# Kernel tuning notes

Measured on AMD Instinct MI355X. Metric: run time of the kernel, lower is better.

The kernel has to match this reference:

```python
import jax, jax.numpy as jnp
import numpy as np
from jax import lax

HIDDEN = 1024
SEQ_NUM = 2048
SEQ_LEN = 10  # hard-coded by input_seq.view(-1, 1, 10) in the torch module


def setup_inputs() -> dict:
    key = jax.random.key(0)
    ks = jax.random.split(key, 7)
    s = 1.0 / np.sqrt(HIDDEN)  # torch RNN/Linear default init scale
    return {
        "input_seq": jax.random.normal(ks[0], (SEQ_NUM, SEQ_LEN), dtype=jnp.float32),
        "W_ih": jax.random.uniform(ks[1], (HIDDEN, 1), jnp.float32, -s, s),
        "b_ih": jax.random.uniform(ks[2], (HIDDEN,), jnp.float32, -s, s),
        "W_hh": jax.random.uniform(ks[3], (HIDDEN, HIDDEN), jnp.float32, -s, s),
        "b_hh": jax.random.uniform(ks[4], (HIDDEN,), jnp.float32, -s, s),
        "W_out": jax.random.uniform(ks[5], (1, HIDDEN), jnp.float32, -s, s),
        "b_out": jax.random.uniform(ks[6], (1,), jnp.float32, -s, s),
    }


def reference(input_seq, W_ih, b_ih, W_hh, b_hh, W_out, b_out):
    # Torch module feeds each scalar of input_seq (viewed as [seqNum,1,10])
    # through nn.RNN one step at a time, carrying hidden_cell across ALL
    # scalars, and applies Linear to the hidden state at every step.
    # h' = tanh(x * w_ih + b_ih + W_hh @ h + b_hh); y = W_out @ h' + b_out
    w_ih = W_ih[:, 0]  # input_size == 1
    xs = input_seq.reshape(-1)  # [T] scalar timesteps, T = seqNum*10

    def step(h, x):
        h_new = jnp.tanh(x * w_ih + b_ih + W_hh @ h + b_hh)
        y = W_out @ h_new + b_out  # [1]
        return h_new, y[0]

    h0 = jnp.zeros((HIDDEN,), dtype=input_seq.dtype)
    _, ys = lax.scan(step, h0, xs)
    return ys.reshape(SEQ_NUM, 1, SEQ_LEN)
```

## Files before the change

kernel.cpp:

```cpp
#include <hip/hip_runtime.h>
#include <math.h>


#define H      1024
#define TSTEPS 20480
#define BLOCK  256
#define WARM   64
#define WGSPC  16

typedef unsigned int uint;
typedef float f32x4 __attribute__((ext_vector_type(4)));

#define HDATA_BYTES ((size_t)64 * 2 * H * sizeof(float))

__device__ __forceinline__ uint f2bf(float f) {
    uint u = __float_as_uint(f);
    return (u + 0x7fffu + ((u >> 16) & 1u)) >> 16;
}

__global__ __launch_bounds__(BLOCK, 1)
void rnn_r22(const float* __restrict__ xs, const float* __restrict__ W_ih,
             const float* __restrict__ b_ih, const float* __restrict__ W_hh,
             const float* __restrict__ b_hh, const float* __restrict__ W_out,
             const float* __restrict__ b_out, float* __restrict__ y,
             float* __restrict__ hdata, uint* __restrict__ ctrl,
             int coop, int ilv, int chunk)
{
    const int tid  = threadIdx.x;
    const int bid  = blockIdx.x;
    const int wave = tid >> 6;
    const int lane = tid & 63;

    __shared__ uint  sW[64][512];
    __shared__ uint  sR[256];
    __shared__ int   sA[3];
    __shared__ float sY[4][4][8];

    uint* rcount = ctrl;
    uint* abortf = ctrl + 16;
    uint* roster = ctrl + 64;
    uint* flbase = ctrl + 1024;

    int group, slot; bool fastm;
    if (coop) {
        uint xcc = __builtin_amdgcn_s_getreg(20 | (31 << 11)) & 7u;
        if (tid == 0) {
            __hip_atomic_store(&roster[bid], xcc, __ATOMIC_RELAXED, __HIP_MEMORY_SCOPE_AGENT);
            asm volatile("s_waitcnt vmcnt(0)" ::: "memory");
            atomicAdd(rcount, 1u);
            while (__hip_atomic_load(rcount, __ATOMIC_RELAXED, __HIP_MEMORY_SCOPE_AGENT) < 256u)
                __builtin_amdgcn_s_sleep(2);
        }
        __syncthreads();
        sR[tid] = __hip_atomic_load(&roster[tid], __ATOMIC_RELAXED, __HIP_MEMORY_SCOPE_AGENT);
        __syncthreads();
        if (tid == 0) {
            int cnt[8] = {0,0,0,0,0,0,0,0};
            int myrank = 0, myx = 0;
            for (int b = 0; b < 256; ++b) {
                int x = (int)(sR[b] & 7u);
                int r = cnt[x]++;
                if (b == bid) { myrank = r; myx = x; }
            }
            int pre[9]; pre[0] = 0;
            for (int x = 0; x < 8; ++x) pre[x + 1] = pre[x] + cnt[x];
            int gidx = pre[myx] + myrank;
            int gr = gidx >> 4, sl = gidx & 15;
            int lo = gr << 4, hi = lo + 16, fok = 0;
            for (int x = 0; x < 8; ++x)
                if (pre[x] <= lo && hi <= pre[x + 1]) fok = 1;
            sA[0] = gr; sA[1] = sl; sA[2] = fok;
        }
        __syncthreads();
        group = sA[0]; slot = sA[1]; fastm = (sA[2] != 0);
    } else {
        group = bid / WGSPC; slot = bid % WGSPC; fastm = false;
    }

    uint* abortp = abortf + group;
    const int wic     = slot * 4 + wave;
    const int rowbase = slot * 64 + wave * 16;
    const int rowwg   = slot * 64;
    const int ck0     = group * ilv;

    for (int idx = tid; idx < 64 * 512; idx += BLOCK) {
        const int r = idx >> 9, p = idx & 511;
        const float2 w = *(const float2*)&W_hh[(size_t)(rowwg + r) * H + 2 * p];
        sW[r][p] = f2bf(w.x) | (f2bf(w.y) << 16);
    }
    __syncthreads();

    const int myrow = rowbase + (lane & 15);
    const float wih_s = W_ih[myrow];
    const float cb_s  = b_ih[myrow] + b_hh[myrow];

    f32x4 wo4[4];
    #pragma unroll
    for (int q = 0; q < 4; ++q)
        wo4[q] = *(const f32x4*)&W_out[256 * q + 4 * lane];
    const float bo = b_out[0];

    int ns[4], t0c[4];
    #pragma unroll
    for (int k = 0; k < 4; ++k) {
        const int ck = ck0 + k;
        const int w_ = (k < ilv && ck) ? WARM : 0;
        ns[k]  = (k < ilv) ? chunk + w_ : 0;
        t0c[k] = ck * chunk - w_;
    }

    f32x4 hrv[4][4] = {};
    float lv0[4] = {0,0,0,0}, lv1[4] = {0,0,0,0};
    uint  lastflag[4] = {0,0,0,0};
    float xcur[4] = {0,0,0,0};
    #pragma unroll
    for (int k = 0; k < 4; ++k)
        if (k < ilv) xcur[k] = xs[t0c[k]];

    auto demote = [&]() {
        #pragma unroll
        for (int k = 0; k < 4; ++k) {
            if (k >= ilv) continue;
            float* hbk = hdata + (size_t)(ck0 + k) * 2 * H;
            float* q0 = hbk + rowbase + (lane & 15);
            float* q1 = q0 + H;
            if (lane < 16) {
                asm volatile("global_store_dword %0, %1, off sc0 sc1"
                             :: "v"(q0), "v"(lv0[k]) : "memory");
                asm volatile("global_store_dword %0, %1, off sc0 sc1"
                             :: "v"(q1), "v"(lv1[k]) : "memory");
            }
            asm volatile("s_waitcnt vmcnt(0)" ::: "memory");
            if (lane == 0)
                asm volatile("global_store_dword %0, %1, off sc0 sc1"
                             :: "v"(flbase + (ck0 + k) * 64 + wic), "v"(lastflag[k]) : "memory");
        }
        asm volatile("s_waitcnt vmcnt(0)" ::: "memory");
        if (lane == 0)
            asm volatile("global_store_dword %0, %1, off sc0 sc1"
                         :: "v"(abortp), "v"(1u) : "memory");
        asm volatile("s_waitcnt vmcnt(0)" ::: "memory");
        fastm = false;
    };

    auto abort_set = [&]() -> bool {
        uint ab;
        asm volatile("global_load_dword %0, %1, off sc0 sc1\n\ts_waitcnt vmcnt(0)"
                     : "=v"(ab) : "v"(abortp) : "memory");
        return __any(ab != 0u);
    };

    auto poll_load_t = [&](int ck, int lt, float* out) {
        const uint* fa = flbase + ck * 64 + lane;
        const uint tt = (uint)lt;
        uint fails = 0;
        for (;;) {
            uint f;
            if (fastm)
                asm volatile("global_load_dword %0, %1, off sc0\n\ts_waitcnt vmcnt(0)"
                             : "=v"(f) : "v"(fa) : "memory");
            else
                asm volatile("global_load_dword %0, %1, off sc0 sc1\n\ts_waitcnt vmcnt(0)"
                             : "=v"(f) : "v"(fa) : "memory");
            if (__all(f >= tt)) break;
            ++fails;
            if (fastm) {
                if ((fails & 63u) == 0u) {
                    if (abort_set() || fails > 8192u) demote();
                }
                __builtin_amdgcn_s_sleep(1);
            } else {
                __builtin_amdgcn_s_sleep(8);
            }
        }
        const float* a = hdata + (size_t)ck * 2 * H + (size_t)(lt & 1) * H + 4 * lane;
        f32x4 A, B, C, D;
        if (fastm)
            asm volatile(
                "global_load_dwordx4 %0, %4, off sc0\n\t"
                "global_load_dwordx4 %1, %4, off offset:1024 sc0\n\t"
                "global_load_dwordx4 %2, %4, off offset:2048 sc0\n\t"
                "global_load_dwordx4 %3, %4, off offset:3072 sc0\n\t"
                "s_waitcnt vmcnt(0)"
                : "=&v"(A), "=&v"(B), "=&v"(C), "=&v"(D) : "v"(a) : "memory");
        else
            asm volatile(
                "global_load_dwordx4 %0, %4, off sc0 sc1\n\t"
                "global_load_dwordx4 %1, %4, off offset:1024 sc0 sc1\n\t"
                "global_load_dwordx4 %2, %4, off offset:2048 sc0 sc1\n\t"
                "global_load_dwordx4 %3, %4, off offset:3072 sc0 sc1\n\t"
                "s_waitcnt vmcnt(0)"
                : "=&v"(A), "=&v"(B), "=&v"(C), "=&v"(D) : "v"(a) : "memory");
        #pragma unroll
        for (int e = 0; e < 4; ++e) {
            out[e] = A[e]; out[4 + e] = B[e]; out[8 + e] = C[e]; out[12 + e] = D[e];
        }
    };

    auto reduce16 = [&](const float* z) -> float {
        float s0,s1,s2,s3,s4,s5,s6,s7;
        {
            const bool b = (lane & 1) != 0;
            s0 = (b ? z[ 1] : z[ 0]) + __shfl_xor(b ? z[ 0] : z[ 1], 1);
            s1 = (b ? z[ 3] : z[ 2]) + __shfl_xor(b ? z[ 2] : z[ 3], 1);
            s2 = (b ? z[ 5] : z[ 4]) + __shfl_xor(b ? z[ 4] : z[ 5], 1);
            s3 = (b ? z[ 7] : z[ 6]) + __shfl_xor(b ? z[ 6] : z[ 7], 1);
            s4 = (b ? z[ 9] : z[ 8]) + __shfl_xor(b ? z[ 8] : z[ 9], 1);
            s5 = (b ? z[11] : z[10]) + __shfl_xor(b ? z[10] : z[11], 1);
            s6 = (b ? z[13] : z[12]) + __shfl_xor(b ? z[12] : z[13], 1);
            s7 = (b ? z[15] : z[14]) + __shfl_xor(b ? z[14] : z[15], 1);
        }
        float t0_,t1_,t2_,t3_;
        {
            const bool b = (lane & 2) != 0;
            t0_ = (b ? s1 : s0) + __shfl_xor(b ? s0 : s1, 2);
            t1_ = (b ? s3 : s2) + __shfl_xor(b ? s2 : s3, 2);
            t2_ = (b ? s5 : s4) + __shfl_xor(b ? s4 : s5, 2);
            t3_ = (b ? s7 : s6) + __shfl_xor(b ? s6 : s7, 2);
        }
        float u0_,u1_;
        {
            const bool b = (lane & 4) != 0;
            u0_ = (b ? t1_ : t0_) + __shfl_xor(b ? t0_ : t1_, 4);
            u1_ = (b ? t3_ : t2_) + __shfl_xor(b ? t2_ : t3_, 4);
        }
        float zr;
        {
            const bool b = (lane & 8) != 0;
            zr = (b ? u1_ : u0_) + __shfl_xor(b ? u0_ : u1_, 8);
        }
        zr += __shfl_xor(zr, 16);
        zr += __shfl_xor(zr, 32);
        return zr;
    };

    auto reduce16x2 = [&](const float* za, const float* zb, float& ra, float& rb) {
        const bool b1 = (lane & 1) != 0;
        float sa0 = (b1 ? za[ 1] : za[ 0]) + __shfl_xor(b1 ? za[ 0] : za[ 1], 1);
        float sb0 = (b1 ? zb[ 1] : zb[ 0]) + __shfl_xor(b1 ? zb[ 0] : zb[ 1], 1);
        float sa1 = (b1 ? za[ 3] : za[ 2]) + __shfl_xor(b1 ? za[ 2] : za[ 3], 1);
        float sb1 = (b1 ? zb[ 3] : zb[ 2]) + __shfl_xor(b1 ? zb[ 2] : zb[ 3], 1);
        float sa2 = (b1 ? za[ 5] : za[ 4]) + __shfl_xor(b1 ? za[ 4] : za[ 5], 1);
        float sb2 = (b1 ? zb[ 5] : zb[ 4]) + __shfl_xor(b1 ? zb[ 4] : zb[ 5], 1);
        float sa3 = (b1 ? za[ 7] : za[ 6]) + __shfl_xor(b1 ? za[ 6] : za[ 7], 1);
        float sb3 = (b1 ? zb[ 7] : zb[ 6]) + __shfl_xor(b1 ? zb[ 6] : zb[ 7], 1);
        float sa4 = (b1 ? za[ 9] : za[ 8]) + __shfl_xor(b1 ? za[ 8] : za[ 9], 1);
        float sb4 = (b1 ? zb[ 9] : zb[ 8]) + __shfl_xor(b1 ? zb[ 8] : zb[ 9], 1);
        float sa5 = (b1 ? za[11] : za[10]) + __shfl_xor(b1 ? za[10] : za[11], 1);
        float sb5 = (b1 ? zb[11] : zb[10]) + __shfl_xor(b1 ? zb[10] : zb[11], 1);
        float sa6 = (b1 ? za[13] : za[12]) + __shfl_xor(b1 ? za[12] : za[13], 1);
        float sb6 = (b1 ? zb[13] : zb[12]) + __shfl_xor(b1 ? zb[12] : zb[13], 1);
        float sa7 = (b1 ? za[15] : za[14]) + __shfl_xor(b1 ? za[14] : za[15], 1);
        float sb7 = (b1 ? zb[15] : zb[14]) + __shfl_xor(b1 ? zb[14] : zb[15], 1);
        const bool b2 = (lane & 2) != 0;
        float ta0 = (b2 ? sa1 : sa0) + __shfl_xor(b2 ? sa0 : sa1, 2);
        float tb0 = (b2 ? sb1 : sb0) + __shfl_xor(b2 ? sb0 : sb1, 2);
        float ta1 = (b2 ? sa3 : sa2) + __shfl_xor(b2 ? sa2 : sa3, 2);
        float tb1 = (b2 ? sb3 : sb2) + __shfl_xor(b2 ? sb2 : sb3, 2);
        float ta2 = (b2 ? sa5 : sa4) + __shfl_xor(b2 ? sa4 : sa5, 2);
        float tb2 = (b2 ? sb5 : sb4) + __shfl_xor(b2 ? sb4 : sb5, 2);
        float ta3 = (b2 ? sa7 : sa6) + __shfl_xor(b2 ? sa6 : sa7, 2);
        float tb3 = (b2 ? sb7 : sb6) + __shfl_xor(b2 ? sb6 : sb7, 2);
        const bool b4 = (lane & 4) != 0;
        float ua0 = (b4 ? ta1 : ta0) + __shfl_xor(b4 ? ta0 : ta1, 4);
        float ub0 = (b4 ? tb1 : tb0) + __shfl_xor(b4 ? tb0 : tb1, 4);
        float ua1 = (b4 ? ta3 : ta2) + __shfl_xor(b4 ? ta2 : ta3, 4);
        float ub1 = (b4 ? tb3 : tb2) + __shfl_xor(b4 ? tb2 : tb3, 4);
        const bool b8 = (lane & 8) != 0;
        float va = (b8 ? ua1 : ua0) + __shfl_xor(b8 ? ua0 : ua1, 8);
        float vb = (b8 ? ub1 : ub0) + __shfl_xor(b8 ? ub0 : ub1, 8);
        va += __shfl_xor(va, 16);
        vb += __shfl_xor(vb, 16);
        va += __shfl_xor(va, 32);
        vb += __shfl_xor(vb, 32);
        ra = va; rb = vb;
    };

    const int nstep_max = chunk + ((ilv > 1 || group) ? WARM : 0);

    #pragma unroll 1
    for (int it = 0; it < nstep_max; ++it) {
        if (fastm && (it & 31) == 1) {
            if (abort_set()) demote();
        }

        float hv[4] = {0, 0, 0, 0};
        #pragma unroll
        for (int kp = 0; kp < 2; ++kp) {
            const int ka = 2 * kp, kb = 2 * kp + 1;
            const bool doa = (ka < ilv) && (it < ns[ka]);
            const bool dob = (kb < ilv) && (it < ns[kb]);
            if (!doa && !dob) continue;
            float za[16], zb[16];
            #pragma unroll
            for (int r = 0; r < 16; ++r) {
                const uint2* wrow = (const uint2*)&sW[wave * 16 + r][2 * lane];
                float a = 0.0f, b = 0.0f;
                #pragma unroll
                for (int q = 0; q < 4; ++q) {
                    const uint2 u = wrow[q * 64];
                    const float w0 = __uint_as_float(u.x << 16);
                    const float w1 = __uint_as_float(u.x & 0xffff0000u);
                    const float w2 = __uint_as_float(u.y << 16);
                    const float w3 = __uint_as_float(u.y & 0xffff0000u);
                    a = fmaf(w0, hrv[ka][q][0], a);
                    b = fmaf(w0, hrv[kb][q][0], b);
                    a = fmaf(w1, hrv[ka][q][1], a);
                    b = fmaf(w1, hrv[kb][q][1], b);
                    a = fmaf(w2, hrv[ka][q][2], a);
                    b = fmaf(w2, hrv[kb][q][2], b);
                    a = fmaf(w3, hrv[ka][q][3], a);
                    b = fmaf(w3, hrv[kb][q][3], b);
                }
                za[r] = a; zb[r] = b;
            }
            float zra, zrb;
            reduce16x2(za, zb, zra, zrb);
            const float va = fmaf(xcur[ka], wih_s, cb_s + zra);
            const float vb = fmaf(xcur[kb], wih_s, cb_s + zrb);
            const float ha = tanhf(va);
            const float hb = tanhf(vb);
            if (doa) hv[ka] = ha;
            if (dob) hv[kb] = hb;
        }

        const int par = (it + 1) & 1;
        #pragma unroll
        for (int k = 0; k < 4; ++k) {
            if (k >= ilv || it >= ns[k]) continue;
            float* dst = hdata + (size_t)((ck0 + k) * 2 + par) * H + rowbase + (lane & 15);
            if (lane < 16) {
                if (fastm)
                    asm volatile("global_store_dword %0, %1, off"
                                 :: "v"(dst), "v"(hv[k]) : "memory");
                else
                    asm volatile("global_store_dword %0, %1, off sc0 sc1"
                                 :: "v"(dst), "v"(hv[k]) : "memory");
            }
        }
        asm volatile("s_waitcnt vmcnt(0)" ::: "memory");
        #pragma unroll
        for (int k = 0; k < 4; ++k) {
            if (k >= ilv || it >= ns[k]) continue;
            const uint nf = (uint)(it + 1);
            if (lane == 0) {
                if (fastm)
                    asm volatile("global_store_dword %0, %1, off"
                                 :: "v"(flbase + (ck0 + k) * 64 + wic), "v"(nf) : "memory");
                else
                    asm volatile("global_store_dword %0, %1, off sc0 sc1"
                                 :: "v"(flbase + (ck0 + k) * 64 + wic), "v"(nf) : "memory");
            }
            if (par == 0) lv0[k] = hv[k]; else lv1[k] = hv[k];
            lastflag[k] = nf;
        }

        #pragma unroll
        for (int k = 0; k < 4; ++k) {
            if (k >= ilv || it >= ns[k]) continue;
            const int warm_k = (ck0 + k) ? WARM : 0;
            if (wic == (it & 63) && it >= warm_k + 1) {
                float acc = 0.0f;
                #pragma unroll
                for (int q = 0; q < 4; ++q) {
                    acc = fmaf(wo4[q][0], hrv[k][q][0], acc);
                    acc = fmaf(wo4[q][1], hrv[k][q][1], acc);
                    acc = fmaf(wo4[q][2], hrv[k][q][2], acc);
                    acc = fmaf(wo4[q][3], hrv[k][q][3], acc);
                }
                #pragma unroll
                for (int off = 32; off > 0; off >>= 1)
                    acc += __shfl_xor(acc, off);
                if (lane == 0) {
                    if (coop) sY[wave][k][it >> 6] = acc + bo;
                    else      y[t0c[k] + it - 1] = acc + bo;
                }
            }
            if (it + 1 < ns[k]) xcur[k] = xs[t0c[k] + it + 1];
        }

        if (ilv == 4) {
            uint tg0 = (it + 1 < ns[0]) ? (uint)(it + 1) : 0u;
            uint tg1 = (it + 1 < ns[1]) ? (uint)(it + 1) : 0u;
            uint tg2 = (it + 1 < ns[2]) ? (uint)(it + 1) : 0u;
            uint tg3 = (it + 1 < ns[3]) ? (uint)(it + 1) : 0u;
            if (tg0 | tg1 | tg2 | tg3) {
                const uint* fa = flbase + ck0 * 64 + lane;
                uint fails = 0;
                for (;;) {
                    uint f0, f1, f2, f3;
                    if (fastm)
                        asm volatile(
                            "global_load_dword %0, %4, off sc0\n\t"
                            "global_load_dword %1, %4, off offset:256 sc0\n\t"
                            "global_load_dword %2, %4, off offset:512 sc0\n\t"
                            "global_load_dword %3, %4, off offset:768 sc0\n\t"
                            "s_waitcnt vmcnt(0)"
                            : "=&v"(f0), "=&v"(f1), "=&v"(f2), "=&v"(f3)
                            : "v"(fa) : "memory");
                    else
                        asm volatile(
                            "global_load_dword %0, %4, off sc0 sc1\n\t"
                            "global_load_dword %1, %4, off offset:256 sc0 sc1\n\t"
                            "global_load_dword %2, %4, off offset:512 sc0 sc1\n\t"
                            "global_load_dword %3, %4, off offset:768 sc0 sc1\n\t"
                            "s_waitcnt vmcnt(0)"
                            : "=&v"(f0), "=&v"(f1), "=&v"(f2), "=&v"(f3)
                            : "v"(fa) : "memory");
                    bool ok = (f0 >= tg0) & (f1 >= tg1) & (f2 >= tg2) & (f3 >= tg3);
                    if (__all(ok)) break;
                    ++fails;
                    if (fastm) {
                        if ((fails & 63u) == 0u) {
                            if (abort_set() || fails > 8192u) demote();
                        }
                        __builtin_amdgcn_s_sleep(1);
                    } else {
                        __builtin_amdgcn_s_sleep(8);
                    }
                }
                const float* a0p = hdata + (size_t)(ck0 * 2 + par) * H + 4 * lane;
                const float* a1p = a0p + 2 * H;
                const float* a2p = a0p + 4 * H;
                const float* a3p = a0p + 6 * H;
                if (fastm)
                    asm volatile(
                        "global_load_dwordx4 %0, %16, off sc0\n\t"
                        "global_load_dwordx4 %1, %16, off offset:1024 sc0\n\t"
                        "global_load_dwordx4 %2, %16, off offset:2048 sc0\n\t"
                        "global_load_dwordx4 %3, %16, off offset:3072 sc0\n\t"
                        "global_load_dwordx4 %4, %17, off sc0\n\t"
                        "global_load_dwordx4 %5, %17, off offset:1024 sc0\n\t"
                        "global_load_dwordx4 %6, %17, off offset:2048 sc0\n\t"
                        "global_load_dwordx4 %7, %17, off offset:3072 sc0\n\t"
                        "global_load_dwordx4 %8, %18, off sc0\n\t"
                        "global_load_dwordx4 %9, %18, off offset:1024 sc0\n\t"
                        "global_load_dwordx4 %10, %18, off offset:2048 sc0\n\t"
                        "global_load_dwordx4 %11, %18, off offset:3072 sc0\n\t"
                        "global_load_dwordx4 %12, %19, off sc0\n\t"
                        "global_load_dwordx4 %13, %19, off offset:1024 sc0\n\t"
                        "global_load_dwordx4 %14, %19, off offset:2048 sc0\n\t"
                        "global_load_dwordx4 %15, %19, off offset:3072 sc0\n\t"
                        "s_waitcnt vmcnt(0)"
                        : "=&v"(hrv[0][0]), "=&v"(hrv[0][1]), "=&v"(hrv[0][2]), "=&v"(hrv[0][3]),
                          "=&v"(hrv[1][0]), "=&v"(hrv[1][1]), "=&v"(hrv[1][2]), "=&v"(hrv[1][3]),
                          "=&v"(hrv[2][0]), "=&v"(hrv[2][1]), "=&v"(hrv[2][2]), "=&v"(hrv[2][3]),
                          "=&v"(hrv[3][0]), "=&v"(hrv[3][1]), "=&v"(hrv[3][2]), "=&v"(hrv[3][3])
                        : "v"(a0p), "v"(a1p), "v"(a2p), "v"(a3p) : "memory");
                else
                    asm volatile(
                        "global_load_dwordx4 %0, %16, off sc0 sc1\n\t"
                        "global_load_dwordx4 %1, %16, off offset:1024 sc0 sc1\n\t"
                        "global_load_dwordx4 %2, %16, off offset:2048 sc0 sc1\n\t"
                        "global_load_dwordx4 %3, %16, off offset:3072 sc0 sc1\n\t"
                        "global_load_dwordx4 %4, %17, off sc0 sc1\n\t"
                        "global_load_dwordx4 %5, %17, off offset:1024 sc0 sc1\n\t"
                        "global_load_dwordx4 %6, %17, off offset:2048 sc0 sc1\n\t"
                        "global_load_dwordx4 %7, %17, off offset:3072 sc0 sc1\n\t"
                        "global_load_dwordx4 %8, %18, off sc0 sc1\n\t"
                        "global_load_dwordx4 %9, %18, off offset:1024 sc0 sc1\n\t"
                        "global_load_dwordx4 %10, %18, off offset:2048 sc0 sc1\n\t"
                        "global_load_dwordx4 %11, %18, off offset:3072 sc0 sc1\n\t"
                        "global_load_dwordx4 %12, %19, off sc0 sc1\n\t"
                        "global_load_dwordx4 %13, %19, off offset:1024 sc0 sc1\n\t"
                        "global_load_dwordx4 %14, %19, off offset:2048 sc0 sc1\n\t"
                        "global_load_dwordx4 %15, %19, off offset:3072 sc0 sc1\n\t"
                        "s_waitcnt vmcnt(0)"
                        : "=&v"(hrv[0][0]), "=&v"(hrv[0][1]), "=&v"(hrv[0][2]), "=&v"(hrv[0][3]),
                          "=&v"(hrv[1][0]), "=&v"(hrv[1][1]), "=&v"(hrv[1][2]), "=&v"(hrv[1][3]),
                          "=&v"(hrv[2][0]), "=&v"(hrv[2][1]), "=&v"(hrv[2][2]), "=&v"(hrv[2][3]),
                          "=&v"(hrv[3][0]), "=&v"(hrv[3][1]), "=&v"(hrv[3][2]), "=&v"(hrv[3][3])
                        : "v"(a0p), "v"(a1p), "v"(a2p), "v"(a3p) : "memory");
            }
        } else {
            if (it + 1 < ns[0]) {
                float out[16];
                poll_load_t(ck0, it + 1, out);
                #pragma unroll
                for (int q = 0; q < 4; ++q)
                    #pragma unroll
                    for (int e = 0; e < 4; ++e)
                        hrv[0][q][e] = out[4 * q + e];
            }
        }
    }

    if (coop) {
        #pragma unroll
        for (int k = 0; k < 4; ++k) {
            if (k >= ilv) continue;
            const int warm_k = (ck0 + k) ? WARM : 0;
            #pragma unroll 1
            for (int kk = 0; kk < 8; ++kk) {
                const int it = (kk << 6) + wic;
                if (it >= warm_k + 1 && it < ns[k] && lane == 0)
                    y[t0c[k] + it - 1] = sY[wave][k][kk];
            }
        }
    }

    if (slot == 0 && wave == 0) {
        #pragma unroll
        for (int k = 0; k < 4; ++k) {
            if (k >= ilv) continue;
            float out[16];
            poll_load_t(ck0 + k, ns[k], out);
            float acc = 0.0f;
            #pragma unroll
            for (int q = 0; q < 4; ++q) {
                acc = fmaf(wo4[q][0], out[4 * q + 0], acc);
                acc = fmaf(wo4[q][1], out[4 * q + 1], acc);
                acc = fmaf(wo4[q][2], out[4 * q + 2], acc);
                acc = fmaf(wo4[q][3], out[4 * q + 3], acc);
            }
            #pragma unroll
            for (int off = 32; off > 0; off >>= 1)
                acc += __shfl_xor(acc, off);
            if (lane == 0) y[t0c[k] + ns[k] - 1] = acc + bo;
        }
    }
}

extern "C" void kernel_launch(void* const* d_in, const int* in_sizes, int n_in,
                              void* d_out, int out_size, void* d_ws, size_t ws_size,
                              hipStream_t stream) {
    const float* xs    = (const float*)d_in[0];
    const float* W_ih  = (const float*)d_in[1];
    const float* b_ih  = (const float*)d_in[2];
    const float* W_hh  = (const float*)d_in[3];
    const float* b_hh  = (const float*)d_in[4];
    const float* W_out = (const float*)d_in[5];
    const float* b_out = (const float*)d_in[6];
    float* y = (float*)d_out;

    const size_t ctrl_bytes = 24576;
    const size_t need = HDATA_BYTES + ctrl_bytes;
    int use_coop = (ws_size >= need) ? 1 : 0;

    float* hdata = (float*)d_ws;
    uint*  ctrl  = (uint*)((char*)d_ws +
                           (use_coop ? HDATA_BYTES
                                     : (size_t)4 * 2 * H * sizeof(float)));

    (void)hipMemsetAsync(d_ws, 0,
                         use_coop ? need
                                  : (size_t)4 * 2 * H * sizeof(float) + ctrl_bytes,
                         stream);

    if (use_coop) {
        int coop = 1, ilv = 4, chunk = TSTEPS / 64;
        void* args[] = { (void*)&xs, (void*)&W_ih, (void*)&b_ih, (void*)&W_hh,
                         (void*)&b_hh, (void*)&W_out, (void*)&b_out, (void*)&y,
                         (void*)&hdata, (void*)&ctrl,
                         (void*)&coop, (void*)&ilv, (void*)&chunk };
        hipError_t e = hipLaunchCooperativeKernel((const void*)rnn_r22,
                                                  dim3(256), dim3(BLOCK),
                                                  args, 0, stream);
        if (e != hipSuccess) use_coop = 0;
    }
    if (!use_coop) {
        rnn_r22<<<4 * WGSPC, BLOCK, 0, stream>>>(
            xs, W_ih, b_ih, W_hh, b_hh, W_out, b_out, y,
            hdata, ctrl, 0, 1, TSTEPS / 4);
    }
}
```

Before: 4.996 ms.

## Double waves per workgroup so each wave owns eight hidden rows

Raises the block size from 256 to 512 threads, giving 8 waves per workgroup, each computing 8 hidden rows instead of 16. The per-wave matvec and shuffle reduction shrink accordingly, shortening the serial critical path of each recurrent step. In exchange there are twice as many per-wave ready flags, so every poll reads two flag words per lane per chunk, and the flag and control region is enlarged to hold them.

```diff
diff --git a/kernel.cpp b/kernel.cpp
--- a/kernel.cpp
+++ b/kernel.cpp
@@ -4,7 +4,7 @@
 
 #define H      1024
 #define TSTEPS 20480
-#define BLOCK  256
+#define BLOCK  512
 #define WARM   64
 #define WGSPC  16
 
@@ -12,6 +12,7 @@
 typedef float f32x4 __attribute__((ext_vector_type(4)));
 
 #define HDATA_BYTES ((size_t)64 * 2 * H * sizeof(float))
+#define CTRL_BYTES  ((size_t)40960)
 
 __device__ __forceinline__ uint f2bf(float f) {
     uint u = __float_as_uint(f);
@@ -19,7 +20,7 @@
 }
 
 __global__ __launch_bounds__(BLOCK, 1)
-void rnn_r22(const float* __restrict__ xs, const float* __restrict__ W_ih,
+void rnn_r23(const float* __restrict__ xs, const float* __restrict__ W_ih,
              const float* __restrict__ b_ih, const float* __restrict__ W_hh,
              const float* __restrict__ b_hh, const float* __restrict__ W_out,
              const float* __restrict__ b_out, float* __restrict__ y,
@@ -34,7 +35,7 @@
     __shared__ uint  sW[64][512];
     __shared__ uint  sR[256];
     __shared__ int   sA[3];
-    __shared__ float sY[4][4][8];
+    __shared__ float sY[8][4][4];
 
     uint* rcount = ctrl;
     uint* abortf = ctrl + 16;
@@ -52,7 +53,8 @@
                 __builtin_amdgcn_s_sleep(2);
         }
         __syncthreads();
-        sR[tid] = __hip_atomic_load(&roster[tid], __ATOMIC_RELAXED, __HIP_MEMORY_SCOPE_AGENT);
+        if (tid < 256)
+            sR[tid] = __hip_atomic_load(&roster[tid], __ATOMIC_RELAXED, __HIP_MEMORY_SCOPE_AGENT);
         __syncthreads();
         if (tid == 0) {
             int cnt[8] = {0,0,0,0,0,0,0,0};
@@ -78,8 +80,8 @@
     }
 
     uint* abortp = abortf + group;
-    const int wic     = slot * 4 + wave;
-    const int rowbase = slot * 64 + wave * 16;
+    const int wic     = slot * 8 + wave;
+    const int rowbase = slot * 64 + wave * 8;
     const int rowwg   = slot * 64;
     const int ck0     = group * ilv;
 
@@ -90,7 +92,7 @@
     }
     __syncthreads();
 
-    const int myrow = rowbase + (lane & 15);
+    const int myrow = rowbase + (lane & 7);
     const float wih_s = W_ih[myrow];
     const float cb_s  = b_ih[myrow] + b_hh[myrow];
 
@@ -122,9 +124,9 @@
         for (int k = 0; k < 4; ++k) {
             if (k >= ilv) continue;
             float* hbk = hdata + (size_t)(ck0 + k) * 2 * H;
-            float* q0 = hbk + rowbase + (lane & 15);
+            float* q0 = hbk + rowbase + (lane & 7);
             float* q1 = q0 + H;
-            if (lane < 16) {
+            if (lane < 8) {
                 asm volatile("global_store_dword %0, %1, off sc0 sc1"
                              :: "v"(q0), "v"(lv0[k]) : "memory");
                 asm volatile("global_store_dword %0, %1, off sc0 sc1"
@@ -133,7 +135,7 @@
             asm volatile("s_waitcnt vmcnt(0)" ::: "memory");
             if (lane == 0)
                 asm volatile("global_store_dword %0, %1, off sc0 sc1"
-                             :: "v"(flbase + (ck0 + k) * 64 + wic), "v"(lastflag[k]) : "memory");
+                             :: "v"(flbase + (ck0 + k) * 128 + wic), "v"(lastflag[k]) : "memory");
         }
         asm volatile("s_waitcnt vmcnt(0)" ::: "memory");
         if (lane == 0)
@@ -151,18 +153,22 @@
     };
 
     auto poll_load_t = [&](int ck, int lt, float* out) {
-        const uint* fa = flbase + ck * 64 + lane;
+        const uint* fa = flbase + ck * 128 + lane;
         const uint tt = (uint)lt;
         uint fails = 0;
         for (;;) {
-            uint f;
+            uint f0, f1;
             if (fastm)
-                asm volatile("global_load_dword %0, %1, off sc0\n\ts_waitcnt vmcnt(0)"
-                             : "=v"(f) : "v"(fa) : "memory");
+                asm volatile("global_load_dword %0, %2, off sc0\n\t"
+                             "global_load_dword %1, %2, off offset:256 sc0\n\t"
+                             "s_waitcnt vmcnt(0)"
+                             : "=&v"(f0), "=&v"(f1) : "v"(fa) : "memory");
             else
-                asm volatile("global_load_dword %0, %1, off sc0 sc1\n\ts_waitcnt vmcnt(0)"
-                             : "=v"(f) : "v"(fa) : "memory");
-            if (__all(f >= tt)) break;
+                asm volatile("global_load_dword %0, %2, off sc0 sc1\n\t"
+                             "global_load_dword %1, %2, off offset:256 sc0 sc1\n\t"
+                             "s_waitcnt vmcnt(0)"
+                             : "=&v"(f0), "=&v"(f1) : "v"(fa) : "memory");
+            if (__all((f0 >= tt) & (f1 >= tt))) break;
             ++fails;
             if (fastm) {
                 if ((fails & 63u) == 0u) {
@@ -197,78 +203,26 @@
         }
     };
 
-    auto reduce16 = [&](const float* z) -> float {
-        float s0,s1,s2,s3,s4,s5,s6,s7;
-        {
-            const bool b = (lane & 1) != 0;
-            s0 = (b ? z[ 1] : z[ 0]) + __shfl_xor(b ? z[ 0] : z[ 1], 1);
-            s1 = (b ? z[ 3] : z[ 2]) + __shfl_xor(b ? z[ 2] : z[ 3], 1);
-            s2 = (b ? z[ 5] : z[ 4]) + __shfl_xor(b ? z[ 4] : z[ 5], 1);
-            s3 = (b ? z[ 7] : z[ 6]) + __shfl_xor(b ? z[ 6] : z[ 7], 1);
-            s4 = (b ? z[ 9] : z[ 8]) + __shfl_xor(b ? z[ 8] : z[ 9], 1);
-            s5 = (b ? z[11] : z[10]) + __shfl_xor(b ? z[10] : z[11], 1);
-            s6 = (b ? z[13] : z[12]) + __shfl_xor(b ? z[12] : z[13], 1);
-            s7 = (b ? z[15] : z[14]) + __shfl_xor(b ? z[14] : z[15], 1);
-        }
-        float t0_,t1_,t2_,t3_;
-        {
-            const bool b = (lane & 2) != 0;
-            t0_ = (b ? s1 : s0) + __shfl_xor(b ? s0 : s1, 2);
-            t1_ = (b ? s3 : s2) + __shfl_xor(b ? s2 : s3, 2);
-            t2_ = (b ? s5 : s4) + __shfl_xor(b ? s4 : s5, 2);
-            t3_ = (b ? s7 : s6) + __shfl_xor(b ? s6 : s7, 2);
-        }
-        float u0_,u1_;
-        {
-            const bool b = (lane & 4) != 0;
-            u0_ = (b ? t1_ : t0_) + __shfl_xor(b ? t0_ : t1_, 4);
-            u1_ = (b ? t3_ : t2_) + __shfl_xor(b ? t2_ : t3_, 4);
-        }
-        float zr;
-        {
-            const bool b = (lane & 8) != 0;
-            zr = (b ? u1_ : u0_) + __shfl_xor(b ? u0_ : u1_, 8);
-        }
-        zr += __shfl_xor(zr, 16);
-        zr += __shfl_xor(zr, 32);
-        return zr;
-    };
-
-    auto reduce16x2 = [&](const float* za, const float* zb, float& ra, float& rb) {
+    auto reduce8x2 = [&](const float* za, const float* zb, float& ra, float& rb) {
         const bool b1 = (lane & 1) != 0;
-        float sa0 = (b1 ? za[ 1] : za[ 0]) + __shfl_xor(b1 ? za[ 0] : za[ 1], 1);
-        float sb0 = (b1 ? zb[ 1] : zb[ 0]) + __shfl_xor(b1 ? zb[ 0] : zb[ 1], 1);
-        float sa1 = (b1 ? za[ 3] : za[ 2]) + __shfl_xor(b1 ? za[ 2] : za[ 3], 1);
-        float sb1 = (b1 ? zb[ 3] : zb[ 2]) + __shfl_xor(b1 ? zb[ 2] : zb[ 3], 1);
-        float sa2 = (b1 ? za[ 5] : za[ 4]) + __shfl_xor(b1 ? za[ 4] : za[ 5], 1);
-        float sb2 = (b1 ? zb[ 5] : zb[ 4]) + __shfl_xor(b1 ? zb[ 4] : zb[ 5], 1);
-        float sa3 = (b1 ? za[ 7] : za[ 6]) + __shfl_xor(b1 ? za[ 6] : za[ 7], 1);
-        float sb3 = (b1 ? zb[ 7] : zb[ 6]) + __shfl_xor(b1 ? zb[ 6] : zb[ 7], 1);
-        float sa4 = (b1 ? za[ 9] : za[ 8]) + __shfl_xor(b1 ? za[ 8] : za[ 9], 1);
-        float sb4 = (b1 ? zb[ 9] : zb[ 8]) + __shfl_xor(b1 ? zb[ 8] : zb[ 9], 1);
-        float sa5 = (b1 ? za[11] : za[10]) + __shfl_xor(b1 ? za[10] : za[11], 1);
-        float sb5 = (b1 ? zb[11] : zb[10]) + __shfl_xor(b1 ? zb[10] : zb[11], 1);
-        float sa6 = (b1 ? za[13] : za[12]) + __shfl_xor(b1 ? za[12] : za[13], 1);
-        float sb6 = (b1 ? zb[13] : zb[12]) + __shfl_xor(b1 ? zb[12] : zb[13], 1);
-        float sa7 = (b1 ? za[15] : za[14]) + __shfl_xor(b1 ? za[14] : za[15], 1);
-        float sb7 = (b1 ? zb[15] : zb[14]) + __shfl_xor(b1 ? zb[14] : zb[15], 1);
+        float sa0 = (b1 ? za[1] : za[0]) + __shfl_xor(b1 ? za[0] : za[1], 1);
+        float sb0 = (b1 ? zb[1] : zb[0]) + __shfl_xor(b1 ? zb[0] : zb[1], 1);
+        float sa1 = (b1 ? za[3] : za[2]) + __shfl_xor(b1 ? za[2] : za[3], 1);
+        float sb1 = (b1 ? zb[3] : zb[2]) + __shfl_xor(b1 ? zb[2] : zb[3], 1);
+        float sa2 = (b1 ? za[5] : za[4]) + __shfl_xor(b1 ? za[4] : za[5], 1);
+        float sb2 = (b1 ? zb[5] : zb[4]) + __shfl_xor(b1 ? zb[4] : zb[5], 1);
+        float sa3 = (b1 ? za[7] : za[6]) + __shfl_xor(b1 ? za[6] : za[7], 1);
+        float sb3 = (b1 ? zb[7] : zb[6]) + __shfl_xor(b1 ? zb[6] : zb[7], 1);
         const bool b2 = (lane & 2) != 0;
         float ta0 = (b2 ? sa1 : sa0) + __shfl_xor(b2 ? sa0 : sa1, 2);
         float tb0 = (b2 ? sb1 : sb0) + __shfl_xor(b2 ? sb0 : sb1, 2);
         float ta1 = (b2 ? sa3 : sa2) + __shfl_xor(b2 ? sa2 : sa3, 2);
         float tb1 = (b2 ? sb3 : sb2) + __shfl_xor(b2 ? sb2 : sb3, 2);
-        float ta2 = (b2 ? sa5 : sa4) + __shfl_xor(b2 ? sa4 : sa5, 2);
-        float tb2 = (b2 ? sb5 : sb4) + __shfl_xor(b2 ? sb4 : sb5, 2);
-        float ta3 = (b2 ? sa7 : sa6) + __shfl_xor(b2 ? sa6 : sa7, 2);
-        float tb3 = (b2 ? sb7 : sb6) + __shfl_xor(b2 ? sb6 : sb7, 2);
         const bool b4 = (lane & 4) != 0;
-        float ua0 = (b4 ? ta1 : ta0) + __shfl_xor(b4 ? ta0 : ta1, 4);
-        float ub0 = (b4 ? tb1 : tb0) + __shfl_xor(b4 ? tb0 : tb1, 4);
-        float ua1 = (b4 ? ta3 : ta2) + __shfl_xor(b4 ? ta2 : ta3, 4);
-        float ub1 = (b4 ? tb3 : tb2) + __shfl_xor(b4 ? tb2 : tb3, 4);
-        const bool b8 = (lane & 8) != 0;
-        float va = (b8 ? ua1 : ua0) + __shfl_xor(b8 ? ua0 : ua1, 8);
-        float vb = (b8 ? ub1 : ub0) + __shfl_xor(b8 ? ub0 : ub1, 8);
+        float va = (b4 ? ta1 : ta0) + __shfl_xor(b4 ? ta0 : ta1, 4);
+        float vb = (b4 ? tb1 : tb0) + __shfl_xor(b4 ? tb0 : tb1, 4);
+        va += __shfl_xor(va, 8);
+        vb += __shfl_xor(vb, 8);
         va += __shfl_xor(va, 16);
         vb += __shfl_xor(vb, 16);
         va += __shfl_xor(va, 32);
@@ -291,10 +245,10 @@
             const bool doa = (ka < ilv) && (it < ns[ka]);
             const bool dob = (kb < ilv) && (it < ns[kb]);
             if (!doa && !dob) continue;
-            float za[16], zb[16];
+            float za[8], zb[8];
             #pragma unroll
-            for (int r = 0; r < 16; ++r) {
-                const uint2* wrow = (const uint2*)&sW[wave * 16 + r][2 * lane];
+            for (int r = 0; r < 8; ++r) {
+                const uint2* wrow = (const uint2*)&sW[wave * 8 + r][2 * lane];
                 float a = 0.0f, b = 0.0f;
                 #pragma unroll
                 for (int q = 0; q < 4; ++q) {
@@ -315,7 +269,7 @@
                 za[r] = a; zb[r] = b;
             }
             float zra, zrb;
-            reduce16x2(za, zb, zra, zrb);
+            reduce8x2(za, zb, zra, zrb);
             const float va = fmaf(xcur[ka], wih_s, cb_s + zra);
             const float vb = fmaf(xcur[kb], wih_s, cb_s + zrb);
             const float ha = tanhf(va);
@@ -328,8 +282,8 @@
         #pragma unroll
         for (int k = 0; k < 4; ++k) {
             if (k >= ilv || it >= ns[k]) continue;
-            float* dst = hdata + (size_t)((ck0 + k) * 2 + par) * H + rowbase + (lane & 15);
-            if (lane < 16) {
+            float* dst = hdata + (size_t)((ck0 + k) * 2 + par) * H + rowbase + (lane & 7);
+            if (lane < 8) {
                 if (fastm)
                     asm volatile("global_store_dword %0, %1, off"
                                  :: "v"(dst), "v"(hv[k]) : "memory");
@@ -346,10 +300,10 @@
             if (lane == 0) {
                 if (fastm)
                     asm volatile("global_store_dword %0, %1, off"
-                                 :: "v"(flbase + (ck0 + k) * 64 + wic), "v"(nf) : "memory");
+                                 :: "v"(flbase + (ck0 + k) * 128 + wic), "v"(nf) : "memory");
                 else
                     asm volatile("global_store_dword %0, %1, off sc0 sc1"
-                                 :: "v"(flbase + (ck0 + k) * 64 + wic), "v"(nf) : "memory");
+                                 :: "v"(flbase + (ck0 + k) * 128 + wic), "v"(nf) : "memory");
             }
             if (par == 0) lv0[k] = hv[k]; else lv1[k] = hv[k];
             lastflag[k] = nf;
@@ -359,7 +313,7 @@
         for (int k = 0; k < 4; ++k) {
             if (k >= ilv || it >= ns[k]) continue;
             const int warm_k = (ck0 + k) ? WARM : 0;
-            if (wic == (it & 63) && it >= warm_k + 1) {
+            if (wic == (it & 127) && it >= warm_k + 1) {
                 float acc = 0.0f;
                 #pragma unroll
                 for (int q = 0; q < 4; ++q) {
@@ -372,7 +326,7 @@
                 for (int off = 32; off > 0; off >>= 1)
                     acc += __shfl_xor(acc, off);
                 if (lane == 0) {
-                    if (coop) sY[wave][k][it >> 6] = acc + bo;
+                    if (coop) sY[wave][k][it >> 7] = acc + bo;
                     else      y[t0c[k] + it - 1] = acc + bo;
                 }
             }
@@ -385,29 +339,40 @@
             uint tg2 = (it + 1 < ns[2]) ? (uint)(it + 1) : 0u;
             uint tg3 = (it + 1 < ns[3]) ? (uint)(it + 1) : 0u;
             if (tg0 | tg1 | tg2 | tg3) {
-                const uint* fa = flbase + ck0 * 64 + lane;
+                const uint* fa = flbase + ck0 * 128 + lane;
                 uint fails = 0;
                 for (;;) {
-                    uint f0, f1, f2, f3;
+                    uint f0a, f0b, f1a, f1b, f2a, f2b, f3a, f3b;
                     if (fastm)
                         asm volatile(
-                            "global_load_dword %0, %4, off sc0\n\t"
-                            "global_load_dword %1, %4, off offset:256 sc0\n\t"
-                            "global_load_dword %2, %4, off offset:512 sc0\n\t"
-                            "global_load_dword %3, %4, off offset:768 sc0\n\t"
+                            "global_load_dword %0, %8, off sc0\n\t"
+                            "global_load_dword %1, %8, off offset:256 sc0\n\t"
+                            "global_load_dword %2, %8, off offset:512 sc0\n\t"
+                            "global_load_dword %3, %8, off offset:768 sc0\n\t"
+                            "global_load_dword %4, %8, off offset:1024 sc0\n\t"
+                            "global_load_dword %5, %8, off offset:1280 sc0\n\t"
+                            "global_load_dword %6, %8, off offset:1536 sc0\n\t"
+                            "global_load_dword %7, %8, off offset:1792 sc0\n\t"
                             "s_waitcnt vmcnt(0)"
-                            : "=&v"(f0), "=&v"(f1), "=&v"(f2), "=&v"(f3)
+                            : "=&v"(f0a), "=&v"(f0b), "=&v"(f1a), "=&v"(f1b),
+                              "=&v"(f2a), "=&v"(f2b), "=&v"(f3a), "=&v"(f3b)
                             : "v"(fa) : "memory");
                     else
                         asm volatile(
-                            "global_load_dword %0, %4, off sc0 sc1\n\t"
-                            "global_load_dword %1, %4, off offset:256 sc0 sc1\n\t"
-                            "global_load_dword %2, %4, off offset:512 sc0 sc1\n\t"
-                            "global_load_dword %3, %4, off offset:768 sc0 sc1\n\t"
+                            "global_load_dword %0, %8, off sc0 sc1\n\t"
+                            "global_load_dword %1, %8, off offset:256 sc0 sc1\n\t"
+                            "global_load_dword %2, %8, off offset:512 sc0 sc1\n\t"
+                            "global_load_dword %3, %8, off offset:768 sc0 sc1\n\t"
+                            "global_load_dword %4, %8, off offset:1024 sc0 sc1\n\t"
+                            "global_load_dword %5, %8, off offset:1280 sc0 sc1\n\t"
+                            "global_load_dword %6, %8, off offset:1536 sc0 sc1\n\t"
+                            "global_load_dword %7, %8, off offset:1792 sc0 sc1\n\t"
                             "s_waitcnt vmcnt(0)"
-                            : "=&v"(f0), "=&v"(f1), "=&v"(f2), "=&v"(f3)
+                            : "=&v"(f0a), "=&v"(f0b), "=&v"(f1a), "=&v"(f1b),
+                              "=&v"(f2a), "=&v"(f2b), "=&v"(f3a), "=&v"(f3b)
                             : "v"(fa) : "memory");
-                    bool ok = (f0 >= tg0) & (f1 >= tg1) & (f2 >= tg2) & (f3 >= tg3);
+                    bool ok = (f0a >= tg0) & (f0b >= tg0) & (f1a >= tg1) & (f1b >= tg1)
+                            & (f2a >= tg2) & (f2b >= tg2) & (f3a >= tg3) & (f3b >= tg3);
                     if (__all(ok)) break;
                     ++fails;
                     if (fastm) {
@@ -491,8 +456,8 @@
             if (k >= ilv) continue;
             const int warm_k = (ck0 + k) ? WARM : 0;
             #pragma unroll 1
-            for (int kk = 0; kk < 8; ++kk) {
-                const int it = (kk << 6) + wic;
+            for (int kk = 0; kk < 4; ++kk) {
+                const int it = (kk << 7) + wic;
                 if (it >= warm_k + 1 && it < ns[k] && lane == 0)
                     y[t0c[k] + it - 1] = sY[wave][k][kk];
             }
@@ -533,8 +498,7 @@
     const float* b_out = (const float*)d_in[6];
     float* y = (float*)d_out;
 
-    const size_t ctrl_bytes = 24576;
-    const size_t need = HDATA_BYTES + ctrl_bytes;
+    const size_t need = HDATA_BYTES + CTRL_BYTES;
     int use_coop = (ws_size >= need) ? 1 : 0;
 
     float* hdata = (float*)d_ws;
@@ -544,7 +508,7 @@
 
     (void)hipMemsetAsync(d_ws, 0,
                          use_coop ? need
-                                  : (size_t)4 * 2 * H * sizeof(float) + ctrl_bytes,
+                                  : (size_t)4 * 2 * H * sizeof(float) + CTRL_BYTES,
                          stream);
 
     if (use_coop) {
@@ -553,13 +517,13 @@
                          (void*)&b_hh, (void*)&W_out, (void*)&b_out, (void*)&y,
                          (void*)&hdata, (void*)&ctrl,
                          (void*)&coop, (void*)&ilv, (void*)&chunk };
-        hipError_t e = hipLaunchCooperativeKernel((const void*)rnn_r22,
+        hipError_t e = hipLaunchCooperativeKernel((const void*)rnn_r23,
                                                   dim3(256), dim3(BLOCK),
                                                   args, 0, stream);
         if (e != hipSuccess) use_coop = 0;
     }
     if (!use_coop) {
-        rnn_r22<<<4 * WGSPC, BLOCK, 0, stream>>>(
+        rnn_r23<<<4 * WGSPC, BLOCK, 0, stream>>>(
             xs, W_ih, b_ih, W_hh, b_hh, W_out, b_out, y,
             hdata, ctrl, 0, 1, TSTEPS / 4);
     }
```

After: 7.288 ms. 1.46x slower.
